# Kernel optimization log

Measured on AMD Instinct MI355X. Metric: run time of the kernel, lower is better.

Reference implementation:

```python
import jax, jax.numpy as jnp
import numpy as np

B, C, T, V, D, H, KT = 64, 3, 256, 21, 128, 4, 9


def _adjacency():
    rng = np.random.default_rng(0)
    Araw = (rng.random((V, V)) < 0.3).astype(np.float32)
    Araw = np.maximum(Araw, Araw.T)
    np.fill_diagonal(Araw, 1.0)
    deg = Araw.sum(1)
    Anorm = Araw / np.sqrt(deg[:, None] * deg[None, :])  # D^-1/2 A D^-1/2
    return Araw.astype(np.float32), Anorm.astype(np.float32)


def setup_inputs() -> dict:
    key = jax.random.key(0)
    ks = jax.random.split(key, 24)
    g = lambda i, shape, sc=0.05: jax.random.normal(ks[i], shape, dtype=jnp.float32) * sc
    Araw, Anorm = _adjacency()
    return {
        'x': jax.random.normal(ks[0], (B, C, T, V), dtype=jnp.float32),
        'coord_w': g(1, (C, D)), 'coord_b': g(2, (D,)),
        'joint_emb': g(3, (V, D)),
        'graph_bias': jnp.asarray(Araw),  # nn.Parameter(A.clone().float())
        'wq': g(4, (D, D)), 'bq': g(5, (D,)),
        'wk': g(6, (D, D)), 'bk': g(7, (D,)),
        'wv': g(8, (D, D)), 'bv': g(9, (D,)),
        'wo': g(10, (D, D)), 'bo': g(11, (D,)),
        'gcn_w1': g(12, (D, D)), 'gcn_b1': g(13, (D,)),
        'tcn_w1': g(14, (D, D, KT, 1)), 'tcn_b1': g(15, (D,)),
        'gcn_w2': g(16, (D, D)), 'gcn_b2': g(17, (D,)),
        'tcn_w2': g(18, (D, D, KT, 1)), 'tcn_b2': g(19, (D,)),
        'A': jnp.asarray(Anorm),  # fixed normalized adjacency buffer
    }


def _stgcn(x, A, gw, gb, tw, tb):
    # x: [B, D, T, V]; spatial graph conv then temporal conv, residual.
    res = x
    y = jnp.einsum('bctv,vw->bctw', x, A)              # neighbor aggregation
    y = jnp.einsum('bctv,dc->bdtv', y, gw) + gb[None, :, None, None]
    y = jax.nn.relu(y)
    y = jax.lax.conv_general_dilated(
        y, tw, window_strides=(1, 1), padding=((KT // 2, KT // 2), (0, 0)),
        dimension_numbers=('NCHW', 'OIHW', 'NCHW'))     # temporal conv, kernel 9
    y = y + tb[None, :, None, None]
    return jax.nn.relu(y + res)


def reference(x, coord_w, coord_b, joint_emb, graph_bias, wq, bq, wk, bk, wv, bv,
              wo, bo, gcn_w1, gcn_b1, tcn_w1, tcn_b1, gcn_w2, gcn_b2, tcn_w2,
              tcn_b2, A):
    b, c, t, v = x.shape
    d = coord_w.shape[1]
    dh = d // H
    scale = jnp.float32(1.0 / np.sqrt(dh))
    coords = x.transpose(0, 2, 3, 1).reshape(b * t, v, c)      # [N, V, 3]
    feat = coords @ coord_w + coord_b + joint_emb              # LearnedJointEncoding
    q = (feat @ wq + bq).reshape(-1, v, H, dh)
    k = (feat @ wk + bk).reshape(-1, v, H, dh)
    val = (feat @ wv + bv).reshape(-1, v, H, dh)
    scores = jnp.einsum('nihd,njhd->nhij', q, k) * scale + graph_bias[None, None]
    attn = jax.nn.softmax(scores, axis=-1)                     # [N, H, V, V]
    out = jnp.einsum('nhij,njhd->nihd', attn, val).reshape(-1, v, d)
    feat = out @ wo + bo
    feat = feat.reshape(b, t, v, d).transpose(0, 3, 1, 2)       # [B, D, T, V]
    feat = _stgcn(feat, A, gcn_w1, gcn_b1, tcn_w1, tcn_b1)
    feat = _stgcn(feat, A, gcn_w2, gcn_b2, tcn_w2, tcn_b2)
    return feat, attn
```

## Files before the change

### kernel.cpp

```cpp
#include <hip/hip_runtime.h>
#include <hip/hip_bf16.h>

typedef __hip_bfloat16 bf16;
typedef __attribute__((ext_vector_type(8))) short short8v;
typedef __attribute__((ext_vector_type(4))) float float4v;

#define BB   64
#define CC   3
#define TLEN 256
#define VJ   21
#define DM   128
#define NH   4
#define DH   32
#define KT   9
#define NFR  (BB*TLEN)
#define MTOK (NFR*VJ)
#define NIN  22


__device__ __forceinline__ float b2f(bf16 x){ return __bfloat162float(x); }
__device__ __forceinline__ bf16  f2b(float x){ return __float2bfloat16(x); }
__device__ __forceinline__ float hb2f(short s){ return __uint_as_float(((unsigned)(unsigned short)s) << 16); }
__device__ __forceinline__ float lo16(unsigned u){ return __uint_as_float(u << 16); }
__device__ __forceinline__ float hi16(unsigned u){ return __uint_as_float(u & 0xffff0000u); }
__device__ __forceinline__ short bf2s(float x){ bf16 h = f2b(x); return *reinterpret_cast<short*>(&h); }

__global__ void detect_dtype(const void* __restrict__ xin, int nus, int* __restrict__ flag){
  const unsigned short* u = (const unsigned short*)xin;
  int lim = nus < 65536 ? nus : 65536;
  int bad = 0;
  for (int k = threadIdx.x; k < lim; k += 256){
    float f = __uint_as_float(((unsigned)u[k]) << 16);
    if (!(fabsf(f) < 1e6f)) bad = 1;
  }
  if (bad) atomicOr(flag, 1);
}

struct ConvArgs { const void* src[NIN]; int off[NIN+1]; };

__global__ void convert_inputs(ConvArgs a, bf16* __restrict__ dst,
                               const int* __restrict__ flag, int total){
  int i = blockIdx.x*256 + threadIdx.x;
  if (i >= total) return;
  bool isf32 = (*flag != 0);
  int k = 0;
  while (i >= a.off[k+1]) ++k;
  int j = i - a.off[k];
  float v;
  if (isf32) v = ((const float*)a.src[k])[j];
  else       v = __uint_as_float(((unsigned)((const unsigned short*)a.src[k])[j]) << 16);
  dst[i] = f2b(v);
}

__global__ void prep_weights(const bf16* __restrict__ wq, const bf16* __restrict__ wk,
                             const bf16* __restrict__ wv, const bf16* __restrict__ wo,
                             const bf16* __restrict__ tw1, const bf16* __restrict__ tw2,
                             bf16* __restrict__ wqT, bf16* __restrict__ wkT,
                             bf16* __restrict__ wvT, bf16* __restrict__ woT,
                             bf16* __restrict__ twT1, bf16* __restrict__ twT2){
  int i = blockIdx.x*256 + threadIdx.x;
  if (i < DM*DM){
    int d = i >> 7, e = i & 127;
    wqT[i] = wq[e*DM + d];
    wkT[i] = wk[e*DM + d];
    wvT[i] = wv[e*DM + d];
    woT[i] = wo[e*DM + d];
  }
  if (i < KT*DM*DM){
    int c = i & 127; int d = (i >> 7) & 127; int tap = i >> 14;
    twT1[i] = tw1[(d*DM + c)*KT + tap];
    twT2[i] = tw2[(d*DM + c)*KT + tap];
  }
}

__global__ __launch_bounds__(512) void qkv_gemm(const bf16* __restrict__ x,
                                                const bf16* __restrict__ cw,
                                                const bf16* __restrict__ cb,
                                                const bf16* __restrict__ je,
                                                const bf16* __restrict__ BtQ,
                                                const bf16* __restrict__ BtK,
                                                const bf16* __restrict__ BtV,
                                                const bf16* __restrict__ bq,
                                                const bf16* __restrict__ bk,
                                                const bf16* __restrict__ bv,
                                                bf16* __restrict__ Oq,
                                                bf16* __restrict__ Ok,
                                                bf16* __restrict__ Ov){
  __shared__ short8v lds[128*16];
  __shared__ float sxf[128][4];
  const int tid = threadIdx.x;
  const int r0  = blockIdx.x*128;
  const int bvi = r0 >> 8;
  const int t0  = r0 & (TLEN-1);
  const int blk_b = bvi / VJ, blk_v = bvi % VJ;
  {
    int tok = tid >> 2, c = tid & 3;
    if (tok < 128 && c < 3)
      sxf[tok][c] = b2f(x[((size_t)(blk_b*CC + c)*TLEN + t0 + tok)*VJ + blk_v]);
  }
  __syncthreads();
  for (int i = tid; i < 128*16; i += 512){
    int row = i >> 4, c0 = i & 15;
    short8v cw0 = *reinterpret_cast<const short8v*>(cw + 0*DM + c0*8);
    short8v cw1 = *reinterpret_cast<const short8v*>(cw + 1*DM + c0*8);
    short8v cw2 = *reinterpret_cast<const short8v*>(cw + 2*DM + c0*8);
    short8v cbv = *reinterpret_cast<const short8v*>(cb + c0*8);
    short8v jev = *reinterpret_cast<const short8v*>(je + blk_v*DM + c0*8);
    float x0 = sxf[row][0], x1 = sxf[row][1], x2 = sxf[row][2];
    short8v out;
    #pragma unroll
    for (int e = 0; e < 8; ++e){
      float f = hb2f(cbv[e]) + hb2f(jev[e]);
      f = fmaf(x0, hb2f(cw0[e]), f);
      f = fmaf(x1, hb2f(cw1[e]), f);
      f = fmaf(x2, hb2f(cw2[e]), f);
      out[e] = bf2s(f);
    }
    lds[row*16 + (c0 ^ (row & 7))] = out;
  }
  __syncthreads();
  const int lane = tid & 63;
  const int wid  = tid >> 6;
  const int rbase = (wid >> 2) * 64;
  const int nt0   = (wid & 3) * 2;
  const int l15 = lane & 15, l4 = lane >> 4;
  #pragma unroll
  for (int w = 0; w < 3; ++w){
    const bf16* Bt  = (w==0) ? BtQ : (w==1) ? BtK : BtV;
    const bf16* bia = (w==0) ? bq  : (w==1) ? bk  : bv;
    bf16*       Out = (w==0) ? Oq  : (w==1) ? Ok  : Ov;
    short8v breg[2][4];
    #pragma unroll
    for (int ntl = 0; ntl < 2; ++ntl)
      #pragma unroll
      for (int ks = 0; ks < 4; ++ks)
        breg[ntl][ks] = *reinterpret_cast<const short8v*>(Bt + ((nt0+ntl)*16 + l15)*DM + ks*32 + l4*8);
    float4v acc[4][2];
    #pragma unroll
    for (int rt = 0; rt < 4; ++rt){ acc[rt][0] = (float4v){0,0,0,0}; acc[rt][1] = (float4v){0,0,0,0}; }
    #pragma unroll
    for (int rt = 0; rt < 4; ++rt){
      const int ldsRow = rbase + rt*16 + l15;
      #pragma unroll
      for (int ks = 0; ks < 4; ++ks){
        short8v a = lds[ldsRow*16 + ((ks*4 + l4) ^ (ldsRow & 7))];
        acc[rt][0] = __builtin_amdgcn_mfma_f32_16x16x32_bf16(a, breg[0][ks], acc[rt][0], 0,0,0);
        acc[rt][1] = __builtin_amdgcn_mfma_f32_16x16x32_bf16(a, breg[1][ks], acc[rt][1], 0,0,0);
      }
    }
    #pragma unroll
    for (int rt = 0; rt < 4; ++rt)
      #pragma unroll
      for (int ntl = 0; ntl < 2; ++ntl){
        int col = (nt0+ntl)*16 + l15;
        float bvv = b2f(bia[col]);
        #pragma unroll
        for (int j = 0; j < 4; ++j)
          Out[(size_t)(r0 + rbase + rt*16 + l4*4 + j)*DM + col] = f2b(acc[rt][ntl][j] + bvv);
      }
  }
}

template<int NTAPS, bool RELU, bool RESID>
__global__ __launch_bounds__(256, 4) void conv_gemm(const bf16* __restrict__ A,
                                                    const bf16* __restrict__ Bt,
                                                    const bf16* __restrict__ bias,
                                                    const bf16* resid,
                                                    bf16* Cout){
  constexpr int HT   = NTAPS/2;
  constexpr int ROWS = 64 + 2*HT;
  __shared__ short8v lds[ROWS*16];
  const int tid = threadIdx.x;
  const int r0  = blockIdx.x*64;
  const int t0  = r0 & (TLEN-1);
  const long mb = r0 - t0;
  for (int i = tid; i < ROWS*16; i += 256){
    int row = i >> 4, c0 = i & 15;
    int t = t0 + row - HT;
    if (t < 0) t = 0;
    if (t > TLEN-1) t = TLEN-1;
    lds[row*16 + (c0 ^ (row & 7))] = *reinterpret_cast<const short8v*>(A + (mb + t)*DM + c0*8);
  }
  __syncthreads();
  const int lane = tid & 63;
  const int wid  = tid >> 6;
  const int nt0  = wid * 2;
  const int l15 = lane & 15, l4 = lane >> 4;
  float4v acc[4][2];
  #pragma unroll
  for (int rt = 0; rt < 4; ++rt){ acc[rt][0] = (float4v){0,0,0,0}; acc[rt][1] = (float4v){0,0,0,0}; }

  #pragma unroll
  for (int tap = 0; tap < NTAPS; ++tap){
    const bf16* Btap = Bt + (size_t)tap*DM*DM;
    short8v breg[2][4];
    #pragma unroll
    for (int ntl = 0; ntl < 2; ++ntl)
      #pragma unroll
      for (int ks = 0; ks < 4; ++ks)
        breg[ntl][ks] = *reinterpret_cast<const short8v*>(Btap + ((nt0+ntl)*16 + l15)*DM + ks*32 + l4*8);
    const int dt = tap - HT;
    #pragma unroll
    for (int rt = 0; rt < 4; ++rt){
      const int tl = rt*16 + l15;
      bool valid = true;
      if (NTAPS > 1){
        int ts = t0 + tl + dt;
        valid = (ts >= 0) && (ts < TLEN);
      }
      const int ldsRow = tl + HT + dt;
      #pragma unroll
      for (int ks = 0; ks < 4; ++ks){
        short8v a = lds[ldsRow*16 + ((ks*4 + l4) ^ (ldsRow & 7))];
        if (NTAPS > 1 && !valid) a = (short8v){0,0,0,0,0,0,0,0};
        acc[rt][0] = __builtin_amdgcn_mfma_f32_16x16x32_bf16(a, breg[0][ks], acc[rt][0], 0,0,0);
        acc[rt][1] = __builtin_amdgcn_mfma_f32_16x16x32_bf16(a, breg[1][ks], acc[rt][1], 0,0,0);
      }
    }
  }
  #pragma unroll
  for (int rt = 0; rt < 4; ++rt){
    #pragma unroll
    for (int ntl = 0; ntl < 2; ++ntl){
      int col = (nt0+ntl)*16 + l15;
      float bv = b2f(bias[col]);
      #pragma unroll
      for (int j = 0; j < 4; ++j){
        size_t idx = (size_t)(r0 + rt*16 + l4*4 + j)*DM + col;
        float val = acc[rt][ntl][j] + bv;
        if (RESID) val += b2f(resid[idx]);
        if (RELU) val = fmaxf(val, 0.f);
        Cout[idx] = f2b(val);
      }
    }
  }
}

__global__ __launch_bounds__(256) void attn_core(const bf16* __restrict__ Q,
                                                 const bf16* __restrict__ K,
                                                 const bf16* __restrict__ V,
                                                 const bf16* __restrict__ gbias,
                                                 const bf16* __restrict__ An,
                                                 const bf16* __restrict__ woT,
                                                 const bf16* __restrict__ bo,
                                                 float* __restrict__ attn_out,
                                                 bf16* __restrict__ feat_out,
                                                 bf16* __restrict__ agg_out){
  const int n = blockIdx.x;
  const int bb = n / TLEN, t = n % TLEN;
  const int tid = threadIdx.x;
  __shared__ bf16 skv[3][VJ][136];
  __shared__ float sc[NH*VJ*VJ];
  __shared__ float rmax[NH*VJ], rinv[NH*VJ];
  __shared__ bf16 sgb[VJ*VJ];
  __shared__ bf16 sAn[VJ*VJ];
  __shared__ short8v sao[32*16];
  __shared__ bf16 sfeat[32][136];

  for (int i = tid; i < VJ*VJ; i += 256){ sgb[i] = gbias[i]; sAn[i] = An[i]; }
  for (int i = tid; i < 32*16; i += 256)
    if ((i >> 4) >= VJ) sao[i] = (short8v){0,0,0,0,0,0,0,0};
  for (int i = tid; i < 3*VJ*16; i += 256){
    int c0 = i & 15; int v = (i >> 4) % VJ; int w = i / (16*VJ);
    size_t m = ((size_t)bb*VJ + v)*TLEN + t;
    const bf16* src = (w==0 ? Q : (w==1 ? K : V)) + m*DM + c0*8;
    *reinterpret_cast<short8v*>(&skv[w][v][c0*8]) = *reinterpret_cast<const short8v*>(src);
  }
  __syncthreads();
  const float scale = 0.17677669529663687f;
  for (int idx = tid; idx < NH*VJ*VJ; idx += 256){
    int j = idx % VJ, i2 = (idx/VJ) % VJ, h = idx/(VJ*VJ);
    const unsigned* qr = reinterpret_cast<const unsigned*>(&skv[0][i2][h*DH]);
    const unsigned* kr = reinterpret_cast<const unsigned*>(&skv[1][j][h*DH]);
    float a = 0.f;
    #pragma unroll
    for (int p = 0; p < DH/2; ++p){
      unsigned qa = qr[p], ka = kr[p];
      a = fmaf(lo16(qa), lo16(ka), a);
      a = fmaf(hi16(qa), hi16(ka), a);
    }
    sc[idx] = a*scale + b2f(sgb[i2*VJ + j]);
  }
  __syncthreads();
  for (int r = tid; r < NH*VJ; r += 256){
    float m = -1e30f;
    for (int j = 0; j < VJ; ++j) m = fmaxf(m, sc[r*VJ + j]);
    float s = 0.f;
    for (int j = 0; j < VJ; ++j) s += __expf(sc[r*VJ + j] - m);
    rmax[r] = m; rinv[r] = 1.0f/s;
  }
  __syncthreads();
  for (int idx = tid; idx < NH*VJ*VJ; idx += 256){
    int r = idx / VJ;
    float e = __expf(sc[idx] - rmax[r]) * rinv[r];
    sc[idx] = e;
    attn_out[(size_t)n*(NH*VJ*VJ) + idx] = e;
  }
  __syncthreads();
  for (int i = tid; i < VJ*(DM/2); i += 256){
    int q2 = i & 63; int v = i >> 6;
    int d0 = q2*2; int h = d0 >> 5;
    const float* pr = &sc[(h*VJ + v)*VJ];
    float a0 = 0.f, a1 = 0.f;
    #pragma unroll
    for (int j = 0; j < VJ; ++j){
      unsigned va = *reinterpret_cast<const unsigned*>(&skv[2][j][d0]);
      float p = pr[j];
      a0 = fmaf(p, lo16(va), a0);
      a1 = fmaf(p, hi16(va), a1);
    }
    unsigned u0 = (unsigned)(unsigned short)bf2s(a0);
    unsigned u1 = (unsigned)(unsigned short)bf2s(a1);
    unsigned* lp = reinterpret_cast<unsigned*>(&sao[v*16 + ((q2 >> 2) ^ (v & 7))]);
    lp[q2 & 3] = u0 | (u1 << 16);
  }
  __syncthreads();
  const int lane = tid & 63;
  const int wid  = tid >> 6;
  const int l15 = lane & 15, l4 = lane >> 4;
  float4v acc[2][2];
  #pragma unroll
  for (int mt = 0; mt < 2; ++mt){ acc[mt][0] = (float4v){0,0,0,0}; acc[mt][1] = (float4v){0,0,0,0}; }
  #pragma unroll
  for (int ks = 0; ks < 4; ++ks){
    short8v bfr[2];
    #pragma unroll
    for (int ct = 0; ct < 2; ++ct)
      bfr[ct] = *reinterpret_cast<const short8v*>(woT + (wid*32 + ct*16 + l15)*DM + ks*32 + l4*8);
    #pragma unroll
    for (int mt = 0; mt < 2; ++mt){
      int row = mt*16 + l15;
      short8v a = sao[row*16 + ((ks*4 + l4) ^ (row & 7))];
      acc[mt][0] = __builtin_amdgcn_mfma_f32_16x16x32_bf16(a, bfr[0], acc[mt][0], 0,0,0);
      acc[mt][1] = __builtin_amdgcn_mfma_f32_16x16x32_bf16(a, bfr[1], acc[mt][1], 0,0,0);
    }
  }
  #pragma unroll
  for (int mt = 0; mt < 2; ++mt){
    #pragma unroll
    for (int ct = 0; ct < 2; ++ct){
      int col = wid*32 + ct*16 + l15;
      float bov = b2f(bo[col]);
      #pragma unroll
      for (int j = 0; j < 4; ++j){
        int row = mt*16 + l4*4 + j;
        float fv = acc[mt][ct][j] + bov;
        sfeat[row][col] = f2b(fv);
        if (row < VJ)
          feat_out[(((size_t)bb*VJ + row)*TLEN + t)*DM + col] = f2b(fv);
      }
    }
  }
  __syncthreads();
  float4v acg[2][2];
  #pragma unroll
  for (int mt = 0; mt < 2; ++mt){ acg[mt][0] = (float4v){0,0,0,0}; acg[mt][1] = (float4v){0,0,0,0}; }
  short8v afr[2];
  #pragma unroll
  for (int mt = 0; mt < 2; ++mt){
    int w = mt*16 + l15;
    #pragma unroll
    for (int e = 0; e < 8; ++e){
      int k = l4*8 + e;
      short vsv = 0;
      if (k < VJ && w < VJ) vsv = *reinterpret_cast<const short*>(&sAn[k*VJ + w]);
      afr[mt][e] = vsv;
    }
  }
  #pragma unroll
  for (int ct = 0; ct < 2; ++ct){
    int d = wid*32 + ct*16 + l15;
    short8v bfr;
    #pragma unroll
    for (int e = 0; e < 8; ++e){
      int k = l4*8 + e;
      bfr[e] = *reinterpret_cast<const short*>(&sfeat[k][d]);
    }
    #pragma unroll
    for (int mt = 0; mt < 2; ++mt)
      acg[mt][ct] = __builtin_amdgcn_mfma_f32_16x16x32_bf16(afr[mt], bfr, acg[mt][ct], 0,0,0);
  }
  #pragma unroll
  for (int mt = 0; mt < 2; ++mt){
    #pragma unroll
    for (int ct = 0; ct < 2; ++ct){
      int col = wid*32 + ct*16 + l15;
      #pragma unroll
      for (int j = 0; j < 4; ++j){
        int w = mt*16 + l4*4 + j;
        if (w < VJ)
          agg_out[(((size_t)bb*VJ + w)*TLEN + t)*DM + col] = f2b(acg[mt][ct][j]);
      }
    }
  }
}

__global__ __launch_bounds__(256) void agg_kernel(const bf16* __restrict__ fin,
                                                  const bf16* __restrict__ An,
                                                  bf16* __restrict__ aout){
  const int n = blockIdx.x;
  const int bb = n / TLEN, t = n % TLEN;
  const int tid = threadIdx.x;
  __shared__ bf16 sx[VJ][136];
  __shared__ float sA[VJ*VJ];
  for (int i = tid; i < VJ*VJ; i += 256) sA[i] = b2f(An[i]);
  for (int i = tid; i < VJ*16; i += 256){
    int c0 = i & 15, v = i >> 4;
    size_t m = ((size_t)bb*VJ + v)*TLEN + t;
    *reinterpret_cast<short8v*>(&sx[v][c0*8]) =
      *reinterpret_cast<const short8v*>(fin + m*DM + c0*8);
  }
  __syncthreads();
  for (int i = tid; i < VJ*16; i += 256){
    int c0 = i & 15, w = i >> 4;
    float acc[8] = {0,0,0,0,0,0,0,0};
    #pragma unroll
    for (int u = 0; u < VJ; ++u){
      float a = sA[u*VJ + w];
      short8v xv = *reinterpret_cast<const short8v*>(&sx[u][c0*8]);
      #pragma unroll
      for (int e = 0; e < 8; ++e) acc[e] = fmaf(a, hb2f(xv[e]), acc[e]);
    }
    short8v out;
    #pragma unroll
    for (int e = 0; e < 8; ++e) out[e] = bf2s(acc[e]);
    size_t m = ((size_t)bb*VJ + w)*TLEN + t;
    *reinterpret_cast<short8v*>(aout + m*DM + c0*8) = out;
  }
}

__global__ __launch_bounds__(256) void transpose_out(const bf16* __restrict__ fin,
                                                     float* __restrict__ fout){
  const int bid = blockIdx.x;
  const int b   = bid >> 5;
  const int rem = bid & 31;
  const int t0  = (rem >> 2) * 32;
  const int d0  = (rem & 3) * 32;
  __shared__ bf16 tile[32][VJ][33];
  const int tid = threadIdx.x;
  for (int idx = tid; idx < 32*VJ*32; idx += 256){
    int dl = idx & 31;
    int v  = (idx >> 5) % VJ;
    int tl = idx / (32*VJ);
    tile[tl][v][dl] = fin[(((size_t)b*VJ + v)*TLEN + t0 + tl)*DM + d0 + dl];
  }
  __syncthreads();
  for (int idx = tid; idx < 32*VJ*32; idx += 256){
    int j  = idx % (32*VJ);
    int dl = idx / (32*VJ);
    int tl = j / VJ, v = j % VJ;
    fout[((size_t)(b*DM + d0 + dl)*TLEN + t0 + tl)*VJ + v] = b2f(tile[tl][v][dl]);
  }
}

extern "C" void kernel_launch(void* const* d_in, const int* in_sizes, int n_in,
                              void* d_out, int out_size, void* d_ws, size_t ws_size,
                              hipStream_t stream){
  const size_t featElems = (size_t)MTOK*DM;
  float* outf    = (float*)d_out;
  float* attnOut = outf + featElems;
  bf16* qbuf = (bf16*)d_out;
  bf16* kbuf = qbuf + featElems;

  char* wp = (char*)d_ws;
  auto alloc = [&](size_t bytes)->char*{ char* p = wp; wp += (bytes + 15) & ~(size_t)15; return p; };
  int*  flag = (int*)alloc(16);
  ConvArgs ca; int total = 0;
  for (int i = 0; i < NIN; ++i){ ca.src[i] = d_in[i]; ca.off[i] = total; total += in_sizes[i]; }
  ca.off[NIN] = total;
  bf16* cin   = (bf16*)alloc((size_t)total*2);
  bf16* wqT   = (bf16*)alloc(DM*DM*2);
  bf16* wkT   = (bf16*)alloc(DM*DM*2);
  bf16* wvT   = (bf16*)alloc(DM*DM*2);
  bf16* woT   = (bf16*)alloc(DM*DM*2);
  bf16* twT1  = (bf16*)alloc(KT*DM*DM*2);
  bf16* twT2  = (bf16*)alloc(KT*DM*DM*2);
  bf16* featA = (bf16*)alloc(featElems*2);
  bf16* bufV  = (bf16*)alloc(featElems*2);
  if ((size_t)(wp - (char*)d_ws) > ws_size) return;

  const bf16* x    = cin + ca.off[0];
  const bf16* cw   = cin + ca.off[1];
  const bf16* cb   = cin + ca.off[2];
  const bf16* je   = cin + ca.off[3];
  const bf16* gbias= cin + ca.off[4];
  const bf16* wq   = cin + ca.off[5];
  const bf16* bq   = cin + ca.off[6];
  const bf16* wk   = cin + ca.off[7];
  const bf16* bk   = cin + ca.off[8];
  const bf16* wv   = cin + ca.off[9];
  const bf16* bv   = cin + ca.off[10];
  const bf16* wo   = cin + ca.off[11];
  const bf16* bo   = cin + ca.off[12];
  const bf16* gw1  = cin + ca.off[13];
  const bf16* gb1  = cin + ca.off[14];
  const bf16* tw1  = cin + ca.off[15];
  const bf16* tb1  = cin + ca.off[16];
  const bf16* gw2  = cin + ca.off[17];
  const bf16* gb2  = cin + ca.off[18];
  const bf16* tw2  = cin + ca.off[19];
  const bf16* tb2  = cin + ca.off[20];
  const bf16* An   = cin + ca.off[21];

  const int GB  = MTOK/128;
  const int GB2 = MTOK/64;
  hipMemsetAsync(flag, 0, sizeof(int), stream);
  detect_dtype<<<1, 256, 0, stream>>>(d_in[0], in_sizes[0], flag);
  convert_inputs<<<(total + 255)/256, 256, 0, stream>>>(ca, cin, flag, total);
  prep_weights<<<(KT*DM*DM + 255)/256, 256, 0, stream>>>(wq, wk, wv, wo, tw1, tw2,
                                                         wqT, wkT, wvT, woT, twT1, twT2);
  qkv_gemm<<<GB, 512, 0, stream>>>(x, cw, cb, je, wqT, wkT, wvT, bq, bk, bv,
                                   qbuf, kbuf, bufV);
  attn_core<<<NFR, 256, 0, stream>>>(qbuf, kbuf, bufV, gbias, An, woT, bo,
                                     attnOut, featA, qbuf);
  conv_gemm<1,true,false><<<GB2, 256, 0, stream>>>(qbuf, gw1, gb1, nullptr, kbuf);
  conv_gemm<9,true,true><<<GB2, 256, 0, stream>>>(kbuf, twT1, tb1, featA, featA);
  agg_kernel<<<NFR, 256, 0, stream>>>(featA, An, qbuf);
  conv_gemm<1,true,false><<<GB2, 256, 0, stream>>>(qbuf, gw2, gb2, nullptr, kbuf);
  conv_gemm<9,true,true><<<GB2, 256, 0, stream>>>(kbuf, twT2, tb2, featA, featA);
  transpose_out<<<BB*(TLEN/32)*(DM/32), 256, 0, stream>>>(featA, outf);
}
```

Before: 1.254 ms.

## Compute attention scores and PV product with MFMA and alias shared memory pool

Replaces the scalar FMA loops for QK^T scores and attention-times-V in attn_core with bf16 MFMA 16x16x32 tiles, one wave per head, staging probabilities in a zero-padded bf16 shared buffer. Shared memory is packed into one aliased pool so later-stage buffers reuse earlier regions, which cuts LDS use per block and may raise occupancy. In exchange, attention probabilities are rounded to bf16 before the PV product, and V and P need padding and zeroing. The strided per-element V reads for the B operand may cause bank conflicts.

```diff
diff --git a/kernel.cpp b/kernel.cpp
--- a/kernel.cpp
+++ b/kernel.cpp
@@ -236,6 +236,7 @@
   }
 }
 
+#define POOLSZ 39936
 __global__ __launch_bounds__(256) void attn_core(const bf16* __restrict__ Q,
                                                  const bf16* __restrict__ K,
                                                  const bf16* __restrict__ V,
@@ -246,40 +247,81 @@
                                                  float* __restrict__ attn_out,
                                                  bf16* __restrict__ feat_out,
                                                  bf16* __restrict__ agg_out){
+  __shared__ __align__(16) char pool[POOLSZ];
+  bf16*  sQ   = (bf16*) (pool + 0);
+  bf16*  sK   = (bf16*) (pool + 5712);
+  bf16*  sV   = (bf16*) (pool + 11424);
+  float* sc   = (float*)(pool + 20128);
+  bf16*  sP   = (bf16*) (pool + 27184);
+  bf16*  sgb  = (bf16*) (pool + 37424);
+  bf16*  sAn  = (bf16*) (pool + 38320);
+  float* rmax = (float*)(pool + 39216);
+  float* rinv = (float*)(pool + 39552);
+  bf16*  sao  = (bf16*) (pool + 0);
+  bf16*  sfeat= (bf16*) (pool + 8704);
+
   const int n = blockIdx.x;
   const int bb = n / TLEN, t = n % TLEN;
   const int tid = threadIdx.x;
-  __shared__ bf16 skv[3][VJ][136];
-  __shared__ float sc[NH*VJ*VJ];
-  __shared__ float rmax[NH*VJ], rinv[NH*VJ];
-  __shared__ bf16 sgb[VJ*VJ];
-  __shared__ bf16 sAn[VJ*VJ];
-  __shared__ short8v sao[32*16];
-  __shared__ bf16 sfeat[32][136];
+  const int lane = tid & 63;
+  const int wid  = tid >> 6;
+  const int l15 = lane & 15, l4 = lane >> 4;
 
   for (int i = tid; i < VJ*VJ; i += 256){ sgb[i] = gbias[i]; sAn[i] = An[i]; }
-  for (int i = tid; i < 32*16; i += 256)
-    if ((i >> 4) >= VJ) sao[i] = (short8v){0,0,0,0,0,0,0,0};
-  for (int i = tid; i < 3*VJ*16; i += 256){
+  for (int i = tid; i < 2*VJ*16; i += 256){
     int c0 = i & 15; int v = (i >> 4) % VJ; int w = i / (16*VJ);
     size_t m = ((size_t)bb*VJ + v)*TLEN + t;
-    const bf16* src = (w==0 ? Q : (w==1 ? K : V)) + m*DM + c0*8;
-    *reinterpret_cast<short8v*>(&skv[w][v][c0*8]) = *reinterpret_cast<const short8v*>(src);
-  }
-  __syncthreads();
+    const bf16* src = (w==0 ? Q : K) + m*DM + c0*8;
+    bf16* dst = (w==0 ? sQ : sK) + v*136 + c0*8;
+    *reinterpret_cast<short8v*>(dst) = *reinterpret_cast<const short8v*>(src);
+  }
+  for (int i = tid; i < 32*16; i += 256){
+    int c0 = i & 15; int v = i >> 4;
+    short8v val = (short8v){0,0,0,0,0,0,0,0};
+    if (v < VJ){
+      size_t m = ((size_t)bb*VJ + v)*TLEN + t;
+      val = *reinterpret_cast<const short8v*>(V + m*DM + c0*8);
+    }
+    *reinterpret_cast<short8v*>(sV + v*136 + c0*8) = val;
+  }
+  for (int i = tid; i < 4*32*40/8; i += 256)
+    reinterpret_cast<short8v*>(sP)[i] = (short8v){0,0,0,0,0,0,0,0};
+  __syncthreads();
+
   const float scale = 0.17677669529663687f;
-  for (int idx = tid; idx < NH*VJ*VJ; idx += 256){
-    int j = idx % VJ, i2 = (idx/VJ) % VJ, h = idx/(VJ*VJ);
-    const unsigned* qr = reinterpret_cast<const unsigned*>(&skv[0][i2][h*DH]);
-    const unsigned* kr = reinterpret_cast<const unsigned*>(&skv[1][j][h*DH]);
-    float a = 0.f;
-    #pragma unroll
-    for (int p = 0; p < DH/2; ++p){
-      unsigned qa = qr[p], ka = kr[p];
-      a = fmaf(lo16(qa), lo16(ka), a);
-      a = fmaf(hi16(qa), hi16(ka), a);
-    }
-    sc[idx] = a*scale + b2f(sgb[i2*VJ + j]);
+  {
+    const int h = wid;
+    short8v aq[2], bk2[2];
+    #pragma unroll
+    for (int mt = 0; mt < 2; ++mt){
+      int i = mt*16 + l15; if (i > VJ-1) i = VJ-1;
+      aq[mt] = *reinterpret_cast<const short8v*>(sQ + i*136 + h*DH + l4*8);
+    }
+    #pragma unroll
+    for (int nt = 0; nt < 2; ++nt){
+      int j = nt*16 + l15; if (j > VJ-1) j = VJ-1;
+      bk2[nt] = *reinterpret_cast<const short8v*>(sK + j*136 + h*DH + l4*8);
+    }
+    float4v cs[2][2];
+    #pragma unroll
+    for (int mt = 0; mt < 2; ++mt)
+      #pragma unroll
+      for (int nt = 0; nt < 2; ++nt){
+        cs[mt][nt] = (float4v){0,0,0,0};
+        cs[mt][nt] = __builtin_amdgcn_mfma_f32_16x16x32_bf16(aq[mt], bk2[nt], cs[mt][nt], 0,0,0);
+      }
+    #pragma unroll
+    for (int mt = 0; mt < 2; ++mt)
+      #pragma unroll
+      for (int nt = 0; nt < 2; ++nt){
+        int j = nt*16 + l15;
+        #pragma unroll
+        for (int jj = 0; jj < 4; ++jj){
+          int i = mt*16 + l4*4 + jj;
+          if (i < VJ && j < VJ)
+            sc[(h*VJ + i)*VJ + j] = cs[mt][nt][jj]*scale + b2f(sgb[i*VJ + j]);
+        }
+      }
   }
   __syncthreads();
   for (int r = tid; r < NH*VJ; r += 256){
@@ -292,32 +334,56 @@
   __syncthreads();
   for (int idx = tid; idx < NH*VJ*VJ; idx += 256){
     int r = idx / VJ;
+    int j = idx % VJ, i2 = r % VJ, h = idx/(VJ*VJ);
     float e = __expf(sc[idx] - rmax[r]) * rinv[r];
-    sc[idx] = e;
     attn_out[(size_t)n*(NH*VJ*VJ) + idx] = e;
-  }
-  __syncthreads();
-  for (int i = tid; i < VJ*(DM/2); i += 256){
-    int q2 = i & 63; int v = i >> 6;
-    int d0 = q2*2; int h = d0 >> 5;
-    const float* pr = &sc[(h*VJ + v)*VJ];
-    float a0 = 0.f, a1 = 0.f;
-    #pragma unroll
-    for (int j = 0; j < VJ; ++j){
-      unsigned va = *reinterpret_cast<const unsigned*>(&skv[2][j][d0]);
-      float p = pr[j];
-      a0 = fmaf(p, lo16(va), a0);
-      a1 = fmaf(p, hi16(va), a1);
-    }
-    unsigned u0 = (unsigned)(unsigned short)bf2s(a0);
-    unsigned u1 = (unsigned)(unsigned short)bf2s(a1);
-    unsigned* lp = reinterpret_cast<unsigned*>(&sao[v*16 + ((q2 >> 2) ^ (v & 7))]);
-    lp[q2 & 3] = u0 | (u1 << 16);
-  }
-  __syncthreads();
-  const int lane = tid & 63;
-  const int wid  = tid >> 6;
-  const int l15 = lane & 15, l4 = lane >> 4;
+    sP[(h*32 + i2)*40 + j] = f2b(e);
+  }
+  __syncthreads();
+  float4v cp[2][2];
+  {
+    const int h = wid;
+    short8v pa[2];
+    #pragma unroll
+    for (int mt = 0; mt < 2; ++mt){
+      int i = mt*16 + l15;
+      pa[mt] = *reinterpret_cast<const short8v*>(sP + (h*32 + i)*40 + l4*8);
+    }
+    short8v bv2[2];
+    #pragma unroll
+    for (int nt = 0; nt < 2; ++nt){
+      #pragma unroll
+      for (int e = 0; e < 8; ++e)
+        bv2[nt][e] = *reinterpret_cast<const short*>(sV + (l4*8 + e)*136 + h*DH + nt*16 + l15);
+    }
+    #pragma unroll
+    for (int mt = 0; mt < 2; ++mt)
+      #pragma unroll
+      for (int nt = 0; nt < 2; ++nt){
+        cp[mt][nt] = (float4v){0,0,0,0};
+        cp[mt][nt] = __builtin_amdgcn_mfma_f32_16x16x32_bf16(pa[mt], bv2[nt], cp[mt][nt], 0,0,0);
+      }
+  }
+  __syncthreads();
+  for (int i = tid; i < (32-VJ)*16; i += 256){
+    int row = VJ + i/16, c0 = i & 15;
+    *reinterpret_cast<short8v*>(sao + row*136 + c0*8) = (short8v){0,0,0,0,0,0,0,0};
+  }
+  {
+    const int h = wid;
+    #pragma unroll
+    for (int mt = 0; mt < 2; ++mt)
+      #pragma unroll
+      for (int nt = 0; nt < 2; ++nt){
+        int d = h*DH + nt*16 + l15;
+        #pragma unroll
+        for (int jj = 0; jj < 4; ++jj){
+          int i = mt*16 + l4*4 + jj;
+          if (i < VJ) sao[i*136 + d] = f2b(cp[mt][nt][jj]);
+        }
+      }
+  }
+  __syncthreads();
   float4v acc[2][2];
   #pragma unroll
   for (int mt = 0; mt < 2; ++mt){ acc[mt][0] = (float4v){0,0,0,0}; acc[mt][1] = (float4v){0,0,0,0}; }
@@ -330,7 +396,7 @@
     #pragma unroll
     for (int mt = 0; mt < 2; ++mt){
       int row = mt*16 + l15;
-      short8v a = sao[row*16 + ((ks*4 + l4) ^ (row & 7))];
+      short8v a = *reinterpret_cast<const short8v*>(sao + row*136 + ks*32 + l4*8);
       acc[mt][0] = __builtin_amdgcn_mfma_f32_16x16x32_bf16(a, bfr[0], acc[mt][0], 0,0,0);
       acc[mt][1] = __builtin_amdgcn_mfma_f32_16x16x32_bf16(a, bfr[1], acc[mt][1], 0,0,0);
     }
@@ -345,7 +411,7 @@
       for (int j = 0; j < 4; ++j){
         int row = mt*16 + l4*4 + j;
         float fv = acc[mt][ct][j] + bov;
-        sfeat[row][col] = f2b(fv);
+        sfeat[row*136 + col] = f2b(fv);
         if (row < VJ)
           feat_out[(((size_t)bb*VJ + row)*TLEN + t)*DM + col] = f2b(fv);
       }
@@ -374,7 +440,7 @@
     #pragma unroll
     for (int e = 0; e < 8; ++e){
       int k = l4*8 + e;
-      bfr[e] = *reinterpret_cast<const short*>(&sfeat[k][d]);
+      bfr[e] = *reinterpret_cast<const short*>(sfeat + k*136 + d);
     }
     #pragma unroll
     for (int mt = 0; mt < 2; ++mt)
```

Result: faster. 1.181 ms, median of 2 (-5.9%).
